# Optimization experiments

Measured on AMD Instinct MI355X. Metric: run time of the kernel, lower is better.

## Reference

```python
import jax, jax.numpy as jnp
import numpy as np

B, S, D = 4, 2048, 768
H = 12
DH = D // H  # 64


def setup_inputs() -> dict:
    key = jax.random.key(0)
    ks = jax.random.split(key, 6)
    scale = 0.02
    return {
        "hidden_states": jax.random.normal(ks[0], (B, S, D), dtype=jnp.float32),
        "Wq": jax.random.normal(ks[1], (D, D), dtype=jnp.float32) * scale,
        "bq": jnp.zeros((D,), dtype=jnp.float32),
        "Wk": jax.random.normal(ks[2], (D, D), dtype=jnp.float32) * scale,
        "bk": jnp.zeros((D,), dtype=jnp.float32),
        "Wv": jax.random.normal(ks[3], (D, D), dtype=jnp.float32) * scale,
        "bv": jnp.zeros((D,), dtype=jnp.float32),
        "Wo": jax.random.normal(ks[4], (D, D), dtype=jnp.float32) * scale,
        "bo": jnp.zeros((D,), dtype=jnp.float32),
        "w_mix": jnp.ones((2,), dtype=jnp.float32),
    }


def reference(hidden_states, Wq, bq, Wk, bk, Wv, bv, Wo, bo, w_mix):
    # Q/K/V projections, then split heads: [B,S,D] -> [B,H,S,DH]
    def split_heads(x):
        return x.reshape(B, S, H, DH).transpose(0, 2, 1, 3)

    q = split_heads(hidden_states @ Wq.T + bq)
    k = split_heads(hidden_states @ Wk.T + bk)
    v = split_heads(hidden_states @ Wv.T + bv)

    # [B,H,S,S] attention scores
    scores = jnp.einsum("bhqd,bhkd->bhqk", q, k) / jnp.sqrt(jnp.float32(DH))

    attn_soft = jax.nn.softmax(scores, axis=-1)
    attn_relu2 = jnp.square(jax.nn.relu(scores))
    mix = jax.nn.softmax(w_mix)  # exp(w)/sum(exp(w))
    attn = attn_soft * mix[0] + attn_relu2 * mix[1]
    # dropout rate 0.0 (inference) -> identity

    ctx = jnp.einsum("bhqk,bhkd->bhqd", attn, v)
    ctx = ctx.transpose(0, 2, 1, 3).reshape(B, S, D)
    out = ctx @ Wo.T + bo
    return out
```

## Files before the change

### kernel.cpp

```cpp
#include <hip/hip_runtime.h>

#define DEV __device__ __forceinline__

typedef __attribute__((ext_vector_type(8))) short short8;
typedef __attribute__((ext_vector_type(4))) float f32x4;
typedef __attribute__((ext_vector_type(2))) unsigned int u32x2;
typedef __attribute__((ext_vector_type(4))) unsigned int u32x4;

constexpr int Dm = 768;
constexpr int Sn = 2048;
constexpr int Bn = 4;
constexpr int Hn = 12;
constexpr int Mn = Bn * Sn;

constexpr float kQScale = 0.18033688011112043f;
constexpr float kR2Fix  = 0.4804530139182014f;

DEV unsigned short f32_to_bf16(float f) {
  unsigned int u = __float_as_uint(f);
  u = (u + 0x7fffu + ((u >> 16) & 1u)) >> 16;
  return (unsigned short)u;
}

DEV unsigned cvt_pk_bf16(float lo, float hi) {
  unsigned d;
  asm("v_cvt_pk_bf16_f32 %0, %1, %2" : "=v"(d) : "v"(lo), "v"(hi));
  return d;
}

DEV f32x4 mfma_bf16(short8 a, short8 b, f32x4 c) {
  return __builtin_amdgcn_mfma_f32_16x16x32_bf16(a, b, c, 0, 0, 0);
}

DEV void gload_lds16(const void* g, void* l) {
  __builtin_amdgcn_global_load_lds(
      (__attribute__((address_space(1))) const unsigned int*)g,
      (__attribute__((address_space(3))) unsigned int*)l, 16, 0, 0);
}

DEV short8 transpose_to_bfrag(unsigned xd0, unsigned xd1, unsigned yd0, unsigned yd1) {
  u32x2 a0 = __builtin_amdgcn_permlane32_swap(xd0, yd0, false, false);
  u32x2 b0 = __builtin_amdgcn_permlane16_swap(a0[0], a0[1], false, false);
  u32x2 a1 = __builtin_amdgcn_permlane32_swap(xd1, yd1, false, false);
  u32x2 b1 = __builtin_amdgcn_permlane16_swap(a1[0], a1[1], false, false);
  u32x4 f = {b0[0], b1[0], b0[1], b1[1]};
  return __builtin_bit_cast(short8, f);
}

__global__ __launch_bounds__(256) void k_cast_hidden(const float* __restrict__ src,
                                                     unsigned short* __restrict__ dst) {
  int i = blockIdx.x * 256 + threadIdx.x;
  float4 v = ((const float4*)src)[i];
  ushort4 o;
  o.x = f32_to_bf16(v.x); o.y = f32_to_bf16(v.y);
  o.z = f32_to_bf16(v.z); o.w = f32_to_bf16(v.w);
  ((ushort4*)dst)[i] = o;
}

__global__ __launch_bounds__(256) void k_cast_w(const float* __restrict__ Wq,
                                                const float* __restrict__ Wk,
                                                const float* __restrict__ Wv,
                                                const float* __restrict__ Wo,
                                                unsigned short* __restrict__ wbf) {
  const float* src = (blockIdx.y == 0) ? Wq : (blockIdx.y == 1) ? Wk
                   : (blockIdx.y == 2) ? Wv : Wo;
  unsigned short* dst = wbf + (size_t)blockIdx.y * (Dm * Dm);
  int i = blockIdx.x * 256 + threadIdx.x;
  float4 v = ((const float4*)src)[i];
  ushort4 o;
  o.x = f32_to_bf16(v.x); o.y = f32_to_bf16(v.y);
  o.z = f32_to_bf16(v.z); o.w = f32_to_bf16(v.w);
  ((ushort4*)dst)[i] = o;
}

__global__ __launch_bounds__(256, 3) void k_gemm_qkv(
    const unsigned short* __restrict__ Abf, const unsigned short* __restrict__ wbf,
    const float* __restrict__ bq, const float* __restrict__ bk, const float* __restrict__ bv,
    unsigned short* __restrict__ Qb, unsigned short* __restrict__ Kb,
    unsigned short* __restrict__ Vt) {
  __shared__ unsigned short Sh[128 * 136];
  unsigned short* As = Sh;
  unsigned short* Bs = Sh + 4096;

  const int tid = threadIdx.x;
  const int wave = tid >> 6, lane = tid & 63;
  const int wm = wave >> 1, wn = wave & 1;
  const int quad = lane >> 4, l16 = lane & 15;
  const int bm = blockIdx.y * 128, bn = blockIdx.x * 128;
  const int z = blockIdx.z;

  const unsigned short* W = wbf + (size_t)z * (Dm * Dm);
  const float* bias = (z == 0) ? bq : ((z == 1) ? bk : bv);

  const int sr = lane >> 2;
  const int sc = (lane & 3) * 8;
  const unsigned short* gA0 = Abf + (size_t)(bm + (wave * 2 + 0) * 16 + sr) * Dm + sc;
  const unsigned short* gA1 = Abf + (size_t)(bm + (wave * 2 + 1) * 16 + sr) * Dm + sc;
  const unsigned short* gB0 = W + (size_t)(bn + (wave * 2 + 0) * 16 + sr) * Dm + sc;
  const unsigned short* gB1 = W + (size_t)(bn + (wave * 2 + 1) * 16 + sr) * Dm + sc;
  unsigned short* lA0 = &As[(wave * 2 + 0) * 512];
  unsigned short* lA1 = &As[(wave * 2 + 1) * 512];
  unsigned short* lB0 = &Bs[(wave * 2 + 0) * 512];
  unsigned short* lB1 = &Bs[(wave * 2 + 1) * 512];

  f32x4 acc[4][4];
#pragma unroll
  for (int i = 0; i < 4; ++i)
#pragma unroll
    for (int j = 0; j < 4; ++j)
#pragma unroll
      for (int r = 0; r < 4; ++r) acc[i][j][r] = 0.f;

  for (int kk = 0; kk < Dm; kk += 32) {
    gload_lds16(gA0 + kk, lA0);
    gload_lds16(gA1 + kk, lA1);
    gload_lds16(gB0 + kk, lB0);
    gload_lds16(gB1 + kk, lB1);
    __syncthreads();
    short8 af[4], bf[4];
#pragma unroll
    for (int mi = 0; mi < 4; ++mi)
      af[mi] = *(const short8*)(&As[(wm * 64 + mi * 16 + l16) * 32 + quad * 8]);
#pragma unroll
    for (int ni = 0; ni < 4; ++ni)
      bf[ni] = *(const short8*)(&Bs[(wn * 64 + ni * 16 + l16) * 32 + quad * 8]);
#pragma unroll
    for (int mi = 0; mi < 4; ++mi)
#pragma unroll
      for (int ni = 0; ni < 4; ++ni)
        acc[mi][ni] = mfma_bf16(af[mi], bf[ni], acc[mi][ni]);
    __syncthreads();
  }

  if (z != 2) {
#pragma unroll
    for (int ni = 0; ni < 4; ++ni) {
      int n = bn + wn * 64 + ni * 16 + l16;
      float bias_v = bias[n];
#pragma unroll
      for (int mi = 0; mi < 4; ++mi) {
#pragma unroll
        for (int r = 0; r < 4; ++r) {
          int m = bm + wm * 64 + mi * 16 + quad * 4 + r;
          float val = acc[mi][ni][r] + bias_v;
          if (z == 0)
            Qb[(size_t)m * Dm + n] = f32_to_bf16(val * kQScale);
          else
            Kb[(size_t)m * Dm + n] = f32_to_bf16(val);
        }
      }
    }
  } else {
#pragma unroll
    for (int ni = 0; ni < 4; ++ni) {
      int nl = wn * 64 + ni * 16 + l16;
      float bias_v = bias[bn + nl];
#pragma unroll
      for (int mi = 0; mi < 4; ++mi) {
#pragma unroll
        for (int r = 0; r < 4; ++r) {
          int ml = wm * 64 + mi * 16 + quad * 4 + r;
          Sh[nl * 136 + ml] = f32_to_bf16(acc[mi][ni][r] + bias_v);
        }
      }
    }
    __syncthreads();
    const int bb = bm >> 11;
    const int s0 = bm & 2047;
    const int j = tid >> 4;
    const int cch = tid & 15;
#pragma unroll
    for (int pass = 0; pass < 8; ++pass) {
      int row = pass * 16 + j;
      int n = bn + row;
      int h2 = n >> 6, dcol = n & 63;
      uint4 v = *(const uint4*)(&Sh[row * 136 + cch * 8]);
      *(uint4*)(&Vt[((size_t)((bb * Hn + h2) * 64 + dcol)) * Sn + s0 + cch * 8]) = v;
    }
  }
}

__global__ __launch_bounds__(256, 2) void k_attn(
    const unsigned short* __restrict__ Qb, const unsigned short* __restrict__ Kb,
    const unsigned short* __restrict__ Vt, const float* __restrict__ wmix,
    unsigned short* __restrict__ Ctx) {
  __shared__ unsigned short Ks[128 * 64];
  __shared__ unsigned short Vs[64 * 128];

  const int tid = threadIdx.x;
  const int wave = tid >> 6, lane = tid & 63;
  const int quad = lane >> 4, l16 = lane & 15;
  const int l8 = l16 & 7;
  const int qt = blockIdx.x;
  const int bh = blockIdx.y;
  const int b = bh / Hn, h = bh % Hn;

  const unsigned short* Qg = Qb + (size_t)(b * Sn + qt * 128) * Dm + h * 64;
  const unsigned short* Kg = Kb + (size_t)(b * Sn) * Dm + h * 64;
  const unsigned short* Vg = Vt + (size_t)bh * 64 * Sn;

  const int krr = lane >> 3, kcc = lane & 7;
  const int kchunk = kcc ^ krr;
  const int vrr = lane >> 4, vcc = lane & 15;

#pragma unroll
  for (int i = 0; i < 4; ++i) {
    int t = wave * 4 + i;
    gload_lds16(Qg + (size_t)(t * 8 + krr) * Dm + kchunk * 8, &Ks[t * 512]);
  }
  __syncthreads();
  short8 qf[2][2];
#pragma unroll
  for (int mi = 0; mi < 2; ++mi)
#pragma unroll
    for (int ks = 0; ks < 2; ++ks)
      qf[mi][ks] = *(const short8*)(
          &Ks[(wave * 32 + mi * 16 + l16) * 64 + (((ks * 4 + quad) ^ l8) << 3)]);
  __syncthreads();

  const f32x4 kZero = {0.f, 0.f, 0.f, 0.f};
  short8 ones;
#pragma unroll
  for (int i = 0; i < 8; ++i) ones[i] = (short)0x3F80;

  f32x4 acc_s[2][4], acc_r2[2][4], lacc[2];
#pragma unroll
  for (int i = 0; i < 2; ++i) {
#pragma unroll
    for (int j = 0; j < 4; ++j)
#pragma unroll
      for (int r = 0; r < 4; ++r) { acc_s[i][j][r] = 0.f; acc_r2[i][j][r] = 0.f; }
#pragma unroll
    for (int r = 0; r < 4; ++r) lacc[i][r] = 0.f;
  }

  for (int kt = 0; kt < 16; ++kt) {
#pragma unroll
    for (int i = 0; i < 4; ++i) {
      int t = wave * 4 + i;
      gload_lds16(Kg + (size_t)(kt * 128 + t * 8 + krr) * Dm + kchunk * 8, &Ks[t * 512]);
    }
#pragma unroll
    for (int i = 0; i < 4; ++i) {
      int t = wave * 4 + i;
      int vrow = t * 4 + vrr;
      int vch = vcc ^ ((4 * i + vrr) & 15);
      gload_lds16(Vg + (size_t)vrow * Sn + kt * 128 + vch * 8, &Vs[t * 512]);
    }
    __syncthreads();

#pragma unroll
    for (int c = 0; c < 4; ++c) {
      short8 kf[2][2];
#pragma unroll
      for (int t2 = 0; t2 < 2; ++t2)
#pragma unroll
        for (int ks = 0; ks < 2; ++ks)
          kf[t2][ks] = *(const short8*)(
              &Ks[((c * 2 + t2) * 16 + l16) * 64 + (((ks * 4 + quad) ^ l8) << 3)]);

      f32x4 sacc[2][2];
#pragma unroll
      for (int mi = 0; mi < 2; ++mi)
#pragma unroll
        for (int t2 = 0; t2 < 2; ++t2)
          sacc[mi][t2] = mfma_bf16(kf[t2][1], qf[mi][1],
                                   mfma_bf16(kf[t2][0], qf[mi][0], kZero));

      short8 vf[4];
#pragma unroll
      for (int nv = 0; nv < 4; ++nv)
        vf[nv] = *(const short8*)(
            &Vs[(nv * 16 + l16) * 128 + (((c * 4 + quad) ^ l16) << 3)]);

#pragma unroll
      for (int mi = 0; mi < 2; ++mi) {
        f32x4 s0 = sacc[mi][0], s1 = sacc[mi][1];
        float p1a[4], p1b[4], p2a[4], p2b[4];
#pragma unroll
        for (int r = 0; r < 4; ++r) {
          p1a[r] = __builtin_amdgcn_exp2f(s0[r]);
          p1b[r] = __builtin_amdgcn_exp2f(s1[r]);
          float t0 = fmaxf(s0[r], 0.f), t1 = fmaxf(s1[r], 0.f);
          p2a[r] = t0 * t0;
          p2b[r] = t1 * t1;
        }
        short8 pf1 = transpose_to_bfrag(cvt_pk_bf16(p1a[0], p1a[1]),
                                        cvt_pk_bf16(p1a[2], p1a[3]),
                                        cvt_pk_bf16(p1b[0], p1b[1]),
                                        cvt_pk_bf16(p1b[2], p1b[3]));
        short8 pf2 = transpose_to_bfrag(cvt_pk_bf16(p2a[0], p2a[1]),
                                        cvt_pk_bf16(p2a[2], p2a[3]),
                                        cvt_pk_bf16(p2b[0], p2b[1]),
                                        cvt_pk_bf16(p2b[2], p2b[3]));
#pragma unroll
        for (int nv = 0; nv < 4; ++nv) {
          acc_s[mi][nv] = mfma_bf16(vf[nv], pf1, acc_s[mi][nv]);
          acc_r2[mi][nv] = mfma_bf16(vf[nv], pf2, acc_r2[mi][nv]);
        }
        lacc[mi] = mfma_bf16(ones, pf1, lacc[mi]);
      }
    }
    __syncthreads();
  }

  float w0 = wmix[0], w1 = wmix[1];
  float e0 = __expf(w0), e1 = __expf(w1);
  float mix0 = e0 / (e0 + e1);
  float mix1 = (e1 / (e0 + e1)) * kR2Fix;

#pragma unroll
  for (int mi = 0; mi < 2; ++mi) {
    float a0 = mix0 / lacc[mi][0];
    int srow = qt * 128 + wave * 32 + mi * 16 + l16;
#pragma unroll
    for (int nv = 0; nv < 4; ++nv) {
      float v0 = fmaf(acc_s[mi][nv][0], a0, mix1 * acc_r2[mi][nv][0]);
      float v1 = fmaf(acc_s[mi][nv][1], a0, mix1 * acc_r2[mi][nv][1]);
      float v2 = fmaf(acc_s[mi][nv][2], a0, mix1 * acc_r2[mi][nv][2]);
      float v3 = fmaf(acc_s[mi][nv][3], a0, mix1 * acc_r2[mi][nv][3]);
      uint2 o;
      o.x = cvt_pk_bf16(v0, v1);
      o.y = cvt_pk_bf16(v2, v3);
      *(uint2*)(&Ctx[(size_t)(b * Sn + srow) * Dm + h * 64 + nv * 16 + quad * 4]) = o;
    }
  }
}

__global__ __launch_bounds__(256, 3) void k_gemm_out(
    const unsigned short* __restrict__ Abf, const unsigned short* __restrict__ W,
    const float* __restrict__ bias, float* __restrict__ out) {
  __shared__ unsigned short As[128 * 32];
  __shared__ unsigned short Bs[128 * 32];

  const int tid = threadIdx.x;
  const int wave = tid >> 6, lane = tid & 63;
  const int wm = wave >> 1, wn = wave & 1;
  const int quad = lane >> 4, l16 = lane & 15;
  const int bm = blockIdx.y * 128, bn = blockIdx.x * 128;

  const int sr = lane >> 2;
  const int sc = (lane & 3) * 8;
  const unsigned short* gA0 = Abf + (size_t)(bm + (wave * 2 + 0) * 16 + sr) * Dm + sc;
  const unsigned short* gA1 = Abf + (size_t)(bm + (wave * 2 + 1) * 16 + sr) * Dm + sc;
  const unsigned short* gB0 = W + (size_t)(bn + (wave * 2 + 0) * 16 + sr) * Dm + sc;
  const unsigned short* gB1 = W + (size_t)(bn + (wave * 2 + 1) * 16 + sr) * Dm + sc;
  unsigned short* lA0 = &As[(wave * 2 + 0) * 512];
  unsigned short* lA1 = &As[(wave * 2 + 1) * 512];
  unsigned short* lB0 = &Bs[(wave * 2 + 0) * 512];
  unsigned short* lB1 = &Bs[(wave * 2 + 1) * 512];

  f32x4 acc[4][4];
#pragma unroll
  for (int i = 0; i < 4; ++i)
#pragma unroll
    for (int j = 0; j < 4; ++j)
#pragma unroll
      for (int r = 0; r < 4; ++r) acc[i][j][r] = 0.f;

  for (int kk = 0; kk < Dm; kk += 32) {
    gload_lds16(gA0 + kk, lA0);
    gload_lds16(gA1 + kk, lA1);
    gload_lds16(gB0 + kk, lB0);
    gload_lds16(gB1 + kk, lB1);
    __syncthreads();
    short8 af[4], bf[4];
#pragma unroll
    for (int mi = 0; mi < 4; ++mi)
      af[mi] = *(const short8*)(&As[(wm * 64 + mi * 16 + l16) * 32 + quad * 8]);
#pragma unroll
    for (int ni = 0; ni < 4; ++ni)
      bf[ni] = *(const short8*)(&Bs[(wn * 64 + ni * 16 + l16) * 32 + quad * 8]);
#pragma unroll
    for (int mi = 0; mi < 4; ++mi)
#pragma unroll
      for (int ni = 0; ni < 4; ++ni)
        acc[mi][ni] = mfma_bf16(af[mi], bf[ni], acc[mi][ni]);
    __syncthreads();
  }

#pragma unroll
  for (int ni = 0; ni < 4; ++ni) {
    int n = bn + wn * 64 + ni * 16 + l16;
    float bias_v = bias[n];
#pragma unroll
    for (int mi = 0; mi < 4; ++mi) {
#pragma unroll
      for (int r = 0; r < 4; ++r) {
        int m = bm + wm * 64 + mi * 16 + quad * 4 + r;
        out[(size_t)m * Dm + n] = acc[mi][ni][r] + bias_v;
      }
    }
  }
}

extern "C" void kernel_launch(void* const* d_in, const int* in_sizes, int n_in,
                              void* d_out, int out_size, void* d_ws, size_t ws_size,
                              hipStream_t stream) {
  const float* hs = (const float*)d_in[0];
  const float* Wq = (const float*)d_in[1];
  const float* bq = (const float*)d_in[2];
  const float* Wk = (const float*)d_in[3];
  const float* bk = (const float*)d_in[4];
  const float* Wv = (const float*)d_in[5];
  const float* bv = (const float*)d_in[6];
  const float* Wo = (const float*)d_in[7];
  const float* bo = (const float*)d_in[8];
  const float* wmix = (const float*)d_in[9];

  unsigned short* hbf = (unsigned short*)d_ws;
  unsigned short* wbf = hbf + (size_t)Mn * Dm;
  unsigned short* Qb  = wbf + (size_t)4 * Dm * Dm;
  unsigned short* Kb  = Qb + (size_t)Mn * Dm;
  unsigned short* Vt  = Kb + (size_t)Mn * Dm;
  unsigned short* Ctx = hbf;

  k_cast_hidden<<<dim3(6144), dim3(256), 0, stream>>>(hs, hbf);
  k_cast_w<<<dim3(576, 4), dim3(256), 0, stream>>>(Wq, Wk, Wv, Wo, wbf);
  k_gemm_qkv<<<dim3(6, 64, 3), dim3(256), 0, stream>>>(hbf, wbf, bq, bk, bv, Qb, Kb, Vt);
  k_attn<<<dim3(16, 48), dim3(256), 0, stream>>>(Qb, Kb, Vt, wmix, Ctx);
  k_gemm_out<<<dim3(6, 64), dim3(256), 0, stream>>>(Ctx, wbf + (size_t)3 * Dm * Dm, bo,
                                                    (float*)d_out);
}
```

Measured before the change: 260.1 us.

## Widen QKV GEMM tile to 128x192 over fused weights and raise attention occupancy

The QKV projection now treats Wq/Wk/Wv as one concatenated 2304-row weight and uses 128x192 output tiles on a 12x64 grid instead of 128x128 tiles with a z dimension, so each A tile is reused across more output columns. The V transpose epilogue is split into two half-tile passes to fit the smaller shared buffer. The attention kernel's launch bounds also go from 2 to 3 blocks per SM, which may limit registers and cause spills. The wider tile raises accumulator register pressure in the GEMM.

```diff
diff --git a/kernel.cpp b/kernel.cpp
--- a/kernel.cpp
+++ b/kernel.cpp
@@ -78,7 +78,7 @@
     const float* __restrict__ bq, const float* __restrict__ bk, const float* __restrict__ bv,
     unsigned short* __restrict__ Qb, unsigned short* __restrict__ Kb,
     unsigned short* __restrict__ Vt) {
-  __shared__ unsigned short Sh[128 * 136];
+  __shared__ unsigned short Sh[96 * 136];
   unsigned short* As = Sh;
   unsigned short* Bs = Sh + 4096;
 
@@ -86,28 +86,28 @@
   const int wave = tid >> 6, lane = tid & 63;
   const int wm = wave >> 1, wn = wave & 1;
   const int quad = lane >> 4, l16 = lane & 15;
-  const int bm = blockIdx.y * 128, bn = blockIdx.x * 128;
-  const int z = blockIdx.z;
-
-  const unsigned short* W = wbf + (size_t)z * (Dm * Dm);
-  const float* bias = (z == 0) ? bq : ((z == 1) ? bk : bv);
+  const int bm = blockIdx.y * 128, bn = blockIdx.x * 192;
+  const int seg = blockIdx.x >> 2;
+  const int nloc0 = (blockIdx.x & 3) * 192;
 
   const int sr = lane >> 2;
   const int sc = (lane & 3) * 8;
   const unsigned short* gA0 = Abf + (size_t)(bm + (wave * 2 + 0) * 16 + sr) * Dm + sc;
   const unsigned short* gA1 = Abf + (size_t)(bm + (wave * 2 + 1) * 16 + sr) * Dm + sc;
-  const unsigned short* gB0 = W + (size_t)(bn + (wave * 2 + 0) * 16 + sr) * Dm + sc;
-  const unsigned short* gB1 = W + (size_t)(bn + (wave * 2 + 1) * 16 + sr) * Dm + sc;
+  const unsigned short* gB0 = wbf + (size_t)(bn + (wave * 3 + 0) * 16 + sr) * Dm + sc;
+  const unsigned short* gB1 = wbf + (size_t)(bn + (wave * 3 + 1) * 16 + sr) * Dm + sc;
+  const unsigned short* gB2 = wbf + (size_t)(bn + (wave * 3 + 2) * 16 + sr) * Dm + sc;
   unsigned short* lA0 = &As[(wave * 2 + 0) * 512];
   unsigned short* lA1 = &As[(wave * 2 + 1) * 512];
-  unsigned short* lB0 = &Bs[(wave * 2 + 0) * 512];
-  unsigned short* lB1 = &Bs[(wave * 2 + 1) * 512];
-
-  f32x4 acc[4][4];
+  unsigned short* lB0 = &Bs[(wave * 3 + 0) * 512];
+  unsigned short* lB1 = &Bs[(wave * 3 + 1) * 512];
+  unsigned short* lB2 = &Bs[(wave * 3 + 2) * 512];
+
+  f32x4 acc[4][6];
 #pragma unroll
   for (int i = 0; i < 4; ++i)
 #pragma unroll
-    for (int j = 0; j < 4; ++j)
+    for (int j = 0; j < 6; ++j)
 #pragma unroll
       for (int r = 0; r < 4; ++r) acc[i][j][r] = 0.f;
 
@@ -116,71 +116,75 @@
     gload_lds16(gA1 + kk, lA1);
     gload_lds16(gB0 + kk, lB0);
     gload_lds16(gB1 + kk, lB1);
-    __syncthreads();
-    short8 af[4], bf[4];
+    gload_lds16(gB2 + kk, lB2);
+    __syncthreads();
+    short8 af[4], bf[6];
 #pragma unroll
     for (int mi = 0; mi < 4; ++mi)
       af[mi] = *(const short8*)(&As[(wm * 64 + mi * 16 + l16) * 32 + quad * 8]);
 #pragma unroll
-    for (int ni = 0; ni < 4; ++ni)
-      bf[ni] = *(const short8*)(&Bs[(wn * 64 + ni * 16 + l16) * 32 + quad * 8]);
+    for (int ni = 0; ni < 6; ++ni)
+      bf[ni] = *(const short8*)(&Bs[(wn * 96 + ni * 16 + l16) * 32 + quad * 8]);
 #pragma unroll
     for (int mi = 0; mi < 4; ++mi)
 #pragma unroll
-      for (int ni = 0; ni < 4; ++ni)
+      for (int ni = 0; ni < 6; ++ni)
         acc[mi][ni] = mfma_bf16(af[mi], bf[ni], acc[mi][ni]);
     __syncthreads();
   }
 
-  if (z != 2) {
-#pragma unroll
-    for (int ni = 0; ni < 4; ++ni) {
-      int n = bn + wn * 64 + ni * 16 + l16;
+  if (seg != 2) {
+    const float* bias = (seg == 0) ? bq : bk;
+    unsigned short* Out = (seg == 0) ? Qb : Kb;
+    const float scale = (seg == 0) ? kQScale : 1.0f;
+#pragma unroll
+    for (int ni = 0; ni < 6; ++ni) {
+      int n = nloc0 + wn * 96 + ni * 16 + l16;
       float bias_v = bias[n];
 #pragma unroll
       for (int mi = 0; mi < 4; ++mi) {
 #pragma unroll
         for (int r = 0; r < 4; ++r) {
           int m = bm + wm * 64 + mi * 16 + quad * 4 + r;
-          float val = acc[mi][ni][r] + bias_v;
-          if (z == 0)
-            Qb[(size_t)m * Dm + n] = f32_to_bf16(val * kQScale);
-          else
-            Kb[(size_t)m * Dm + n] = f32_to_bf16(val);
+          Out[(size_t)m * Dm + n] = f32_to_bf16((acc[mi][ni][r] + bias_v) * scale);
         }
       }
     }
   } else {
-#pragma unroll
-    for (int ni = 0; ni < 4; ++ni) {
-      int nl = wn * 64 + ni * 16 + l16;
-      float bias_v = bias[bn + nl];
-#pragma unroll
-      for (int mi = 0; mi < 4; ++mi) {
-#pragma unroll
-        for (int r = 0; r < 4; ++r) {
-          int ml = wm * 64 + mi * 16 + quad * 4 + r;
-          Sh[nl * 136 + ml] = f32_to_bf16(acc[mi][ni][r] + bias_v);
-        }
-      }
-    }
-    __syncthreads();
     const int bb = bm >> 11;
     const int s0 = bm & 2047;
     const int j = tid >> 4;
     const int cch = tid & 15;
 #pragma unroll
-    for (int pass = 0; pass < 8; ++pass) {
-      int row = pass * 16 + j;
-      int n = bn + row;
-      int h2 = n >> 6, dcol = n & 63;
-      uint4 v = *(const uint4*)(&Sh[row * 136 + cch * 8]);
-      *(uint4*)(&Vt[((size_t)((bb * Hn + h2) * 64 + dcol)) * Sn + s0 + cch * 8]) = v;
-    }
-  }
-}
-
-__global__ __launch_bounds__(256, 2) void k_attn(
+    for (int p = 0; p < 2; ++p) {
+      if (wn == p) {
+#pragma unroll
+        for (int ni = 0; ni < 6; ++ni) {
+          int nl = ni * 16 + l16;
+          float bias_v = bv[nloc0 + p * 96 + nl];
+#pragma unroll
+          for (int mi = 0; mi < 4; ++mi)
+#pragma unroll
+            for (int r = 0; r < 4; ++r)
+              Sh[nl * 136 + wm * 64 + mi * 16 + quad * 4 + r] =
+                  f32_to_bf16(acc[mi][ni][r] + bias_v);
+        }
+      }
+      __syncthreads();
+#pragma unroll
+      for (int it = 0; it < 6; ++it) {
+        int row = it * 16 + j;
+        int nv = nloc0 + p * 96 + row;
+        int h2 = nv >> 6, dcol = nv & 63;
+        uint4 v = *(const uint4*)(&Sh[row * 136 + cch * 8]);
+        *(uint4*)(&Vt[((size_t)((bb * Hn + h2) * 64 + dcol)) * Sn + s0 + cch * 8]) = v;
+      }
+      __syncthreads();
+    }
+  }
+}
+
+__global__ __launch_bounds__(256, 3) void k_attn(
     const unsigned short* __restrict__ Qb, const unsigned short* __restrict__ Kb,
     const unsigned short* __restrict__ Vt, const float* __restrict__ wmix,
     unsigned short* __restrict__ Ctx) {
@@ -417,7 +421,7 @@
 
   k_cast_hidden<<<dim3(6144), dim3(256), 0, stream>>>(hs, hbf);
   k_cast_w<<<dim3(576, 4), dim3(256), 0, stream>>>(Wq, Wk, Wv, Wo, wbf);
-  k_gemm_qkv<<<dim3(6, 64, 3), dim3(256), 0, stream>>>(hbf, wbf, bq, bk, bv, Qb, Kb, Vt);
+  k_gemm_qkv<<<dim3(12, 64), dim3(256), 0, stream>>>(hbf, wbf, bq, bk, bv, Qb, Kb, Vt);
   k_attn<<<dim3(16, 48), dim3(256), 0, stream>>>(Qb, Kb, Vt, wmix, Ctx);
   k_gemm_out<<<dim3(6, 64), dim3(256), 0, stream>>>(Ctx, wbf + (size_t)3 * Dm * Dm, bo,
                                                     (float*)d_out);
```

New measurement: 259.3 us. No clear change (-0.3%).
